# Kernel optimization log

Hardware: AMD Instinct MI355X
Metric: run time of the kernel (lower is better)

Reference implementation:

```python
import jax, jax.numpy as jnp
import numpy as np

IN_FEAT, HIDDEN, OUT_FEAT = 2048, 1024, 2048
CODEBOOK_DIM, NUM_CODES = 32, 256
B, S = 4, 4096


def setup_inputs() -> dict:
    key = jax.random.key(0)
    ks = jax.random.split(key, 10)
    sc = lambda fan_in: 1.0 / np.sqrt(fan_in)
    return {
        "x": jax.random.normal(ks[0], (B, S, IN_FEAT), dtype=jnp.float32),
        # down: Linear(in_feat, hidden)
        "down_w": jax.random.normal(ks[1], (HIDDEN, IN_FEAT), dtype=jnp.float32) * sc(IN_FEAT),
        "down_b": jax.random.normal(ks[2], (HIDDEN,), dtype=jnp.float32) * sc(IN_FEAT),
        # VQ project_in: Linear(hidden, codebook_dim)
        "pin_w": jax.random.normal(ks[3], (CODEBOOK_DIM, HIDDEN), dtype=jnp.float32) * sc(HIDDEN),
        "pin_b": jax.random.normal(ks[4], (CODEBOOK_DIM,), dtype=jnp.float32) * sc(HIDDEN),
        # codebook embeddings
        "codebook": jax.random.normal(ks[5], (NUM_CODES, CODEBOOK_DIM), dtype=jnp.float32),
        # VQ project_out: Linear(codebook_dim, hidden)
        "pout_w": jax.random.normal(ks[6], (HIDDEN, CODEBOOK_DIM), dtype=jnp.float32) * sc(CODEBOOK_DIM),
        "pout_b": jax.random.normal(ks[7], (HIDDEN,), dtype=jnp.float32) * sc(CODEBOOK_DIM),
        # up: Linear(hidden, out_feat)
        "up_w": jax.random.normal(ks[8], (OUT_FEAT, HIDDEN), dtype=jnp.float32) * sc(HIDDEN),
        "up_b": jax.random.normal(ks[9], (OUT_FEAT,), dtype=jnp.float32) * sc(HIDDEN),
    }


def reference(x, down_w, down_b, pin_w, pin_b, codebook, pout_w, pout_b, up_w, up_b):
    # down-proj: [B,S,in] -> [B,S,hidden]
    h = jnp.einsum("bsi,hi->bsh", x, down_w) + down_b
    # VQ project_in: [B,S,hidden] -> [B,S,codebook_dim]
    z = jnp.einsum("bsh,ch->bsc", h, pin_w) + pin_b
    # squared euclidean distances to codebook: [B,S,num_codes]
    dist = (
        jnp.sum(z * z, axis=-1, keepdims=True)
        - 2.0 * jnp.einsum("bsc,nc->bsn", z, codebook)
        + jnp.sum(codebook * codebook, axis=-1)
    )
    indices = jnp.argmin(dist, axis=-1)  # [B,S] int
    quant = codebook[indices]            # [B,S,codebook_dim]
    # straight-through estimator
    quant = z + jax.lax.stop_gradient(quant - z)
    # VQ project_out: -> [B,S,hidden]
    hq = jnp.einsum("bsc,hc->bsh", quant, pout_w) + pout_b
    # up-proj: -> [B,S,out]
    out = jnp.einsum("bsh,oh->bso", hq, up_w) + up_b
    commit_loss = jnp.zeros((), dtype=x.dtype)  # commitment_weight = 0
    return jnp.clip(out, -1.0, 1.0), indices, commit_loss
```

## Files before the change

### kernel.cpp

```cpp
#include <hip/hip_runtime.h>

#define TOK   16384
#define INFT  2048
#define HID   1024
#define CBD   32
#define NC    256
#define OUTF  2048
#define KB    4

#define WS_UPWT   0
#define WS_ZPART  0
#define WS_PART   2097152
#define WS_WFT    3145728
#define WS_U2C    3211264
#define WS_BF     3276800
#define WS_BPART  3278880
#define WS_T      3311648
#define WS_IDX    3835936

__global__ void kt_transpose(const float* __restrict__ up_w, float* __restrict__ up_wT) {
    __shared__ float tile[32][33];
    int h0 = blockIdx.x * 32;
    int o0 = blockIdx.y * 32;
    int tx = threadIdx.x & 31, ty = threadIdx.x >> 5;
    #pragma unroll
    for (int j = 0; j < 32; j += 8)
        tile[ty + j][tx] = up_w[(o0 + ty + j) * HID + h0 + tx];
    __syncthreads();
    #pragma unroll
    for (int j = 0; j < 32; j += 8)
        up_wT[(h0 + ty + j) * OUTF + o0 + tx] = tile[tx][ty + j];
}

__global__ void k_fuse_partial(const float* __restrict__ lhs, const float* __restrict__ rhs,
                               float* __restrict__ part, int lhsSC, int lhsSK) {
    int i  = blockIdx.x * 256 + threadIdx.x;
    int k0 = blockIdx.y * 64;
    float acc[32];
    #pragma unroll
    for (int c = 0; c < 32; c++) acc[c] = 0.f;
    #pragma unroll 4
    for (int j = 0; j < 64; j++) {
        float xv = rhs[(k0 + j) * 2048 + i];
        #pragma unroll
        for (int c = 0; c < 32; c++)
            acc[c] = fmaf(lhs[c * lhsSC + (k0 + j) * lhsSK], xv, acc[c]);
    }
    #pragma unroll
    for (int c = 0; c < 32; c++)
        part[(blockIdx.y * 32 + c) * 2048 + i] = acc[c];
}

__global__ void k_fuse_reduce(const float* __restrict__ part, float* __restrict__ outw,
                              int outSI, int outSC) {
    int f = blockIdx.x * 256 + threadIdx.x;
    int i = f & 2047, c = f >> 11;
    float s = 0.f;
    #pragma unroll
    for (int b = 0; b < 16; b++) s += part[b * 65536 + c * 2048 + i];
    outw[i * outSI + c * outSC] = s;
}

__global__ void k_bias_f(const float* __restrict__ pin_w, const float* __restrict__ pin_b,
                         const float* __restrict__ down_b, float* __restrict__ bf) {
    __shared__ float red[256];
    int c = threadIdx.x >> 3, seg = threadIdx.x & 7;
    float s = 0.f;
    #pragma unroll 8
    for (int k = seg * 128; k < seg * 128 + 128; k++)
        s = fmaf(pin_w[c * HID + k], down_b[k], s);
    red[threadIdx.x] = s;
    __syncthreads();
    if (threadIdx.x < 32) {
        float t = pin_b[threadIdx.x];
        #pragma unroll
        for (int q = 0; q < 8; q++) t += red[threadIdx.x * 8 + q];
        bf[threadIdx.x] = t;
    }
}

__global__ void k_bias2_part(const float* __restrict__ up_wT, const float* __restrict__ pout_b,
                             const float* __restrict__ up_b, float* __restrict__ bpart) {
    int o  = blockIdx.x * 256 + threadIdx.x;
    int hc = blockIdx.y;
    float s = (hc == 0) ? up_b[o] : 0.f;
    #pragma unroll 8
    for (int h = hc * 64; h < hc * 64 + 64; h++)
        s = fmaf(up_wT[h * 2048 + o], pout_b[h], s);
    bpart[hc * 2048 + o] = s;
}

__global__ void k_table(const float* __restrict__ U2c, const float* __restrict__ cb,
                        const float* __restrict__ bpart, float* __restrict__ T) {
    int n = blockIdx.x;
    int o = blockIdx.y * 256 + threadIdx.x;
    float s = 0.f;
    #pragma unroll
    for (int hc = 0; hc < 16; hc++) s += bpart[hc * 2048 + o];
    #pragma unroll
    for (int c = 0; c < 32; c++)
        s = fmaf(cb[n * 32 + c], U2c[c * 2048 + o], s);
    T[n * 2048 + o] = s;
}

__global__ __launch_bounds__(256) void k_zpart(const float* __restrict__ x,
                                               const float* __restrict__ WfT,
                                               float* __restrict__ zpart) {
    __shared__ float4 xs[64 * 33 + 1];
    int tid  = threadIdx.x;
    int lane = tid & 63;
    int w    = __builtin_amdgcn_readfirstlane(tid >> 6);
    int m0   = blockIdx.x * 64;
    int kb   = blockIdx.y;

    float acc[32];
    #pragma unroll
    for (int c = 0; c < 32; c++) acc[c] = 0.f;

    for (int sc = 0; sc < 4; sc++) {
        int k0 = kb * 512 + sc * 128;
        #pragma unroll
        for (int j = 0; j < 8; j++) {
            int f = j * 256 + tid;
            int t = f >> 5, q = f & 31;
            xs[t * 33 + q] = *(const float4*)(x + (size_t)(m0 + t) * 2048 + k0 + q * 4);
        }
        __syncthreads();
        const float* wr = WfT + (size_t)(k0 + w * 32) * 32;
        #pragma unroll 2
        for (int j = 0; j < 8; j++) {
            float4 xv = xs[lane * 33 + w * 8 + j];
            #pragma unroll
            for (int c = 0; c < 32; c++) {
                acc[c] = fmaf(wr[(j * 4 + 0) * 32 + c], xv.x, acc[c]);
                acc[c] = fmaf(wr[(j * 4 + 1) * 32 + c], xv.y, acc[c]);
                acc[c] = fmaf(wr[(j * 4 + 2) * 32 + c], xv.z, acc[c]);
                acc[c] = fmaf(wr[(j * 4 + 3) * 32 + c], xv.w, acc[c]);
            }
        }
        __syncthreads();
    }

    float* rp = (float*)xs;
    #pragma unroll
    for (int c = 0; c < 32; c++)
        rp[(w * 64 + lane) * 33 + c] = acc[c];
    __syncthreads();
    int t  = tid >> 2;
    int cq = (tid & 3) * 8;
    float s[8];
    #pragma unroll
    for (int j = 0; j < 8; j++) {
        float v = rp[(0 * 64 + t) * 33 + cq + j];
        #pragma unroll
        for (int ww = 1; ww < 4; ww++) v += rp[(ww * 64 + t) * 33 + cq + j];
        s[j] = v;
    }
    float* zp = zpart + ((size_t)kb * TOK + m0 + t) * 32 + cq;
    *(float4*)zp       = make_float4(s[0], s[1], s[2], s[3]);
    *(float4*)(zp + 4) = make_float4(s[4], s[5], s[6], s[7]);
}

__global__ __launch_bounds__(256) void k_zred(
    const float* __restrict__ zpart, const float* __restrict__ bf,
    const float* __restrict__ cb,
    int* __restrict__ idx_i, float* __restrict__ idx_f) {
    __shared__ float z_s[64 * 36];
    __shared__ float cbs[256 * 36];
    __shared__ float cbn[256];
    __shared__ float red_d[256];
    __shared__ int   red_i[256];

    int tid  = threadIdx.x;
    int lane = tid & 63;
    int w    = __builtin_amdgcn_readfirstlane(tid >> 6);
    int m0   = blockIdx.x * 64;

    #pragma unroll
    for (int i = 0; i < 8; i++) {
        int f = i * 256 + tid;
        int t = f >> 5, c = f & 31;
        float s = bf[c];
        #pragma unroll
        for (int kb = 0; kb < KB; kb++)
            s += zpart[((size_t)kb * TOK + m0 + t) * 32 + c];
        z_s[t * 36 + c] = s;
    }
    #pragma unroll
    for (int j = 0; j < 8; j++) {
        int f = j * 256 + tid;
        int n = f >> 3, q = f & 7;
        float4 v = *(const float4*)(cb + n * 32 + q * 4);
        cbs[n * 36 + q * 4 + 0] = v.x;
        cbs[n * 36 + q * 4 + 1] = v.y;
        cbs[n * 36 + q * 4 + 2] = v.z;
        cbs[n * 36 + q * 4 + 3] = v.w;
    }
    __syncthreads();
    {
        float s = 0.f;
        #pragma unroll
        for (int q = 0; q < 8; q++) {
            float4 v = *(const float4*)(&cbs[tid * 36 + q * 4]);
            s += v.x * v.x + v.y * v.y + v.z * v.z + v.w * v.w;
        }
        cbn[tid] = s;
    }
    __syncthreads();

    float z[32];
    #pragma unroll
    for (int q = 0; q < 8; q++) {
        float4 v = *(const float4*)(&z_s[lane * 36 + q * 4]);
        z[q * 4 + 0] = v.x; z[q * 4 + 1] = v.y; z[q * 4 + 2] = v.z; z[q * 4 + 3] = v.w;
    }
    float bd = 3.4e38f; int bi = 0;
    for (int t = 0; t < 64; t++) {
        int n = w * 64 + t;
        float s = 0.f;
        #pragma unroll
        for (int q = 0; q < 8; q++) {
            float4 v = *(const float4*)(&cbs[n * 36 + q * 4]);
            s = fmaf(v.x, z[q * 4 + 0], s);
            s = fmaf(v.y, z[q * 4 + 1], s);
            s = fmaf(v.z, z[q * 4 + 2], s);
            s = fmaf(v.w, z[q * 4 + 3], s);
        }
        float d = fmaf(-2.f, s, cbn[n]);
        if (d < bd) { bd = d; bi = n; }
    }
    red_d[w * 64 + lane] = bd;
    red_i[w * 64 + lane] = bi;
    __syncthreads();
    if (tid < 64) {
        float d0 = red_d[tid]; int i0 = red_i[tid];
        #pragma unroll
        for (int ww = 1; ww < 4; ww++) {
            float d1 = red_d[ww * 64 + tid];
            int   i1 = red_i[ww * 64 + tid];
            if (d1 < d0) { d0 = d1; i0 = i1; }
        }
        idx_i[m0 + tid] = i0;
        idx_f[m0 + tid] = (float)i0;
    }
}

__global__ void k_gather(const float* __restrict__ T, const int* __restrict__ idx_i,
                         float* __restrict__ out, float* __restrict__ loss) {
    int m   = blockIdx.x * 2 + (threadIdx.x >> 7);
    int sub = threadIdx.x & 127;
    int n = idx_i[m];
    const float4* Tr = (const float4*)(T + (size_t)n * 2048);
    float4* Or = (float4*)(out + (size_t)m * 2048);
    #pragma unroll
    for (int j = 0; j < 4; j++) {
        float4 v = Tr[j * 128 + sub];
        v.x = fminf(fmaxf(v.x, -1.f), 1.f);
        v.y = fminf(fmaxf(v.y, -1.f), 1.f);
        v.z = fminf(fmaxf(v.z, -1.f), 1.f);
        v.w = fminf(fmaxf(v.w, -1.f), 1.f);
        Or[j * 128 + sub] = v;
    }
    if (blockIdx.x == 0 && threadIdx.x == 0) *loss = 0.f;
}

extern "C" void kernel_launch(void* const* d_in, const int* in_sizes, int n_in,
                              void* d_out, int out_size, void* d_ws, size_t ws_size,
                              hipStream_t stream) {
    const float* x      = (const float*)d_in[0];
    const float* down_w = (const float*)d_in[1];
    const float* down_b = (const float*)d_in[2];
    const float* pin_w  = (const float*)d_in[3];
    const float* pin_b  = (const float*)d_in[4];
    const float* cb     = (const float*)d_in[5];
    const float* pout_w = (const float*)d_in[6];
    const float* pout_b = (const float*)d_in[7];
    const float* up_w   = (const float*)d_in[8];
    const float* up_b   = (const float*)d_in[9];

    float* ws    = (float*)d_ws;
    float* up_wT = ws + WS_UPWT;
    float* zpart = ws + WS_ZPART;
    float* part  = ws + WS_PART;
    float* WfT   = ws + WS_WFT;
    float* U2c   = ws + WS_U2C;
    float* bf    = ws + WS_BF;
    float* bpart = ws + WS_BPART;
    float* T     = ws + WS_T;
    int*   idx   = (int*)(ws + WS_IDX);

    float* out_f  = (float*)d_out;
    float* idx_f  = out_f + (size_t)TOK * OUTF;
    float* loss_f = idx_f + TOK;

    kt_transpose<<<dim3(32, 64), 256, 0, stream>>>(up_w, up_wT);
    k_fuse_partial<<<dim3(8, 16), 256, 0, stream>>>(pin_w, down_w, part, HID, 1);
    k_fuse_reduce<<<256, 256, 0, stream>>>(part, WfT, 32, 1);
    k_bias_f<<<1, 256, 0, stream>>>(pin_w, pin_b, down_b, bf);
    k_fuse_partial<<<dim3(8, 16), 256, 0, stream>>>(pout_w, up_wT, part, 1, CBD);
    k_fuse_reduce<<<256, 256, 0, stream>>>(part, U2c, 1, 2048);
    k_bias2_part<<<dim3(8, 16), 256, 0, stream>>>(up_wT, pout_b, up_b, bpart);
    k_table<<<dim3(256, 8), 256, 0, stream>>>(U2c, cb, bpart, T);

    k_zpart<<<dim3(256, KB), 256, 0, stream>>>(x, WfT, zpart);
    k_zred<<<256, 256, 0, stream>>>(zpart, bf, cb, idx, idx_f);
    k_gather<<<8192, 256, 0, stream>>>(T, idx, out_f, loss_f);
}
```

Before: 456.8 us.

## Merge eleven launches into four stages with block-range dispatch and fused gather

```diff
diff --git a/kernel.cpp b/kernel.cpp
--- a/kernel.cpp
+++ b/kernel.cpp
@@ -10,166 +10,209 @@
 
 #define WS_UPWT   0
 #define WS_ZPART  0
-#define WS_PART   2097152
+#define WS_PART1  2097152
+#define WS_T      2097152
 #define WS_WFT    3145728
-#define WS_U2C    3211264
-#define WS_BF     3276800
-#define WS_BPART  3278880
-#define WS_T      3311648
-#define WS_IDX    3835936
-
-__global__ void kt_transpose(const float* __restrict__ up_w, float* __restrict__ up_wT) {
-    __shared__ float tile[32][33];
-    int h0 = blockIdx.x * 32;
-    int o0 = blockIdx.y * 32;
-    int tx = threadIdx.x & 31, ty = threadIdx.x >> 5;
-    #pragma unroll
-    for (int j = 0; j < 32; j += 8)
-        tile[ty + j][tx] = up_w[(o0 + ty + j) * HID + h0 + tx];
-    __syncthreads();
-    #pragma unroll
-    for (int j = 0; j < 32; j += 8)
-        up_wT[(h0 + ty + j) * OUTF + o0 + tx] = tile[tx][ty + j];
-}
-
-__global__ void k_fuse_partial(const float* __restrict__ lhs, const float* __restrict__ rhs,
-                               float* __restrict__ part, int lhsSC, int lhsSK) {
-    int i  = blockIdx.x * 256 + threadIdx.x;
-    int k0 = blockIdx.y * 64;
-    float acc[32];
-    #pragma unroll
-    for (int c = 0; c < 32; c++) acc[c] = 0.f;
-    #pragma unroll 4
-    for (int j = 0; j < 64; j++) {
-        float xv = rhs[(k0 + j) * 2048 + i];
+#define WS_BF     3211264
+#define WS_BPART  3211296
+#define WS_PART2  3311648
+
+__global__ __launch_bounds__(256) void k_stage1(
+    const float* __restrict__ up_w, const float* __restrict__ pin_w,
+    const float* __restrict__ pin_b, const float* __restrict__ down_w,
+    const float* __restrict__ down_b, float* __restrict__ ws) {
+    int bid = blockIdx.x, tid = threadIdx.x;
+    if (bid < 2048) {
+        __shared__ float tile[32][33];
+        float* up_wT = ws + WS_UPWT;
+        int h0 = (bid & 31) * 32;
+        int o0 = (bid >> 5) * 32;
+        int tx = tid & 31, ty = tid >> 5;
+        #pragma unroll
+        for (int j = 0; j < 32; j += 8)
+            tile[ty + j][tx] = up_w[(o0 + ty + j) * HID + h0 + tx];
+        __syncthreads();
+        #pragma unroll
+        for (int j = 0; j < 32; j += 8)
+            up_wT[(h0 + ty + j) * OUTF + o0 + tx] = tile[tx][ty + j];
+    } else if (bid < 2176) {
+        float* part1 = ws + WS_PART1;
+        int b  = bid - 2048;
+        int i  = (b & 7) * 256 + tid;
+        int k0 = (b >> 3) * 64;
+        float acc[32];
+        #pragma unroll
+        for (int c = 0; c < 32; c++) acc[c] = 0.f;
+        #pragma unroll 4
+        for (int j = 0; j < 64; j++) {
+            float xv = down_w[(k0 + j) * 2048 + i];
+            #pragma unroll
+            for (int c = 0; c < 32; c++)
+                acc[c] = fmaf(pin_w[c * HID + k0 + j], xv, acc[c]);
+        }
         #pragma unroll
         for (int c = 0; c < 32; c++)
-            acc[c] = fmaf(lhs[c * lhsSC + (k0 + j) * lhsSK], xv, acc[c]);
-    }
-    #pragma unroll
-    for (int c = 0; c < 32; c++)
-        part[(blockIdx.y * 32 + c) * 2048 + i] = acc[c];
-}
-
-__global__ void k_fuse_reduce(const float* __restrict__ part, float* __restrict__ outw,
-                              int outSI, int outSC) {
-    int f = blockIdx.x * 256 + threadIdx.x;
-    int i = f & 2047, c = f >> 11;
-    float s = 0.f;
-    #pragma unroll
-    for (int b = 0; b < 16; b++) s += part[b * 65536 + c * 2048 + i];
-    outw[i * outSI + c * outSC] = s;
-}
-
-__global__ void k_bias_f(const float* __restrict__ pin_w, const float* __restrict__ pin_b,
-                         const float* __restrict__ down_b, float* __restrict__ bf) {
-    __shared__ float red[256];
-    int c = threadIdx.x >> 3, seg = threadIdx.x & 7;
-    float s = 0.f;
-    #pragma unroll 8
-    for (int k = seg * 128; k < seg * 128 + 128; k++)
-        s = fmaf(pin_w[c * HID + k], down_b[k], s);
-    red[threadIdx.x] = s;
-    __syncthreads();
-    if (threadIdx.x < 32) {
-        float t = pin_b[threadIdx.x];
-        #pragma unroll
-        for (int q = 0; q < 8; q++) t += red[threadIdx.x * 8 + q];
-        bf[threadIdx.x] = t;
-    }
-}
-
-__global__ void k_bias2_part(const float* __restrict__ up_wT, const float* __restrict__ pout_b,
-                             const float* __restrict__ up_b, float* __restrict__ bpart) {
-    int o  = blockIdx.x * 256 + threadIdx.x;
-    int hc = blockIdx.y;
-    float s = (hc == 0) ? up_b[o] : 0.f;
-    #pragma unroll 8
-    for (int h = hc * 64; h < hc * 64 + 64; h++)
-        s = fmaf(up_wT[h * 2048 + o], pout_b[h], s);
-    bpart[hc * 2048 + o] = s;
-}
-
-__global__ void k_table(const float* __restrict__ U2c, const float* __restrict__ cb,
-                        const float* __restrict__ bpart, float* __restrict__ T) {
-    int n = blockIdx.x;
-    int o = blockIdx.y * 256 + threadIdx.x;
-    float s = 0.f;
-    #pragma unroll
-    for (int hc = 0; hc < 16; hc++) s += bpart[hc * 2048 + o];
-    #pragma unroll
-    for (int c = 0; c < 32; c++)
-        s = fmaf(cb[n * 32 + c], U2c[c * 2048 + o], s);
-    T[n * 2048 + o] = s;
-}
-
-__global__ __launch_bounds__(256) void k_zpart(const float* __restrict__ x,
-                                               const float* __restrict__ WfT,
-                                               float* __restrict__ zpart) {
+            part1[((b >> 3) * 32 + c) * 2048 + i] = acc[c];
+    } else {
+        __shared__ float red[256];
+        float* bf = ws + WS_BF;
+        int c = tid >> 3, seg = tid & 7;
+        float s = 0.f;
+        #pragma unroll 8
+        for (int k = seg * 128; k < seg * 128 + 128; k++)
+            s = fmaf(pin_w[c * HID + k], down_b[k], s);
+        red[tid] = s;
+        __syncthreads();
+        if (tid < 32) {
+            float t = pin_b[tid];
+            #pragma unroll
+            for (int q = 0; q < 8; q++) t += red[tid * 8 + q];
+            bf[tid] = t;
+        }
+    }
+}
+
+__global__ __launch_bounds__(256) void k_stage2(
+    const float* __restrict__ pout_w, const float* __restrict__ pout_b,
+    const float* __restrict__ up_b, float* __restrict__ ws) {
+    int bid = blockIdx.x, tid = threadIdx.x;
+    if (bid < 256) {
+        const float* part1 = ws + WS_PART1;
+        float* WfT = ws + WS_WFT;
+        int f = bid * 256 + tid;
+        int i = f & 2047, c = f >> 11;
+        float s = 0.f;
+        #pragma unroll
+        for (int b = 0; b < 16; b++) s += part1[b * 65536 + c * 2048 + i];
+        WfT[i * 32 + c] = s;
+    } else {
+        const float* up_wT = ws + WS_UPWT;
+        float* part2 = ws + WS_PART2;
+        float* bpart = ws + WS_BPART;
+        int b  = bid - 256;
+        int i  = (b & 7) * 256 + tid;
+        int hc = b >> 3;
+        int k0 = hc * 128;
+        float acc[32];
+        #pragma unroll
+        for (int c = 0; c < 32; c++) acc[c] = 0.f;
+        float accb = 0.f;
+        #pragma unroll 4
+        for (int j = 0; j < 128; j++) {
+            float xv = up_wT[(k0 + j) * 2048 + i];
+            accb = fmaf(pout_b[k0 + j], xv, accb);
+            #pragma unroll
+            for (int c = 0; c < 32; c++)
+                acc[c] = fmaf(pout_w[(k0 + j) * 32 + c], xv, acc[c]);
+        }
+        #pragma unroll
+        for (int c = 0; c < 32; c++)
+            part2[(hc * 32 + c) * 2048 + i] = acc[c];
+        bpart[hc * 2048 + i] = accb + (hc == 0 ? up_b[i] : 0.f);
+    }
+}
+
+__global__ __launch_bounds__(256) void k_stage3(
+    const float* __restrict__ x, const float* __restrict__ cb,
+    float* __restrict__ ws) {
     __shared__ float4 xs[64 * 33 + 1];
-    int tid  = threadIdx.x;
-    int lane = tid & 63;
-    int w    = __builtin_amdgcn_readfirstlane(tid >> 6);
-    int m0   = blockIdx.x * 64;
-    int kb   = blockIdx.y;
-
-    float acc[32];
-    #pragma unroll
-    for (int c = 0; c < 32; c++) acc[c] = 0.f;
-
-    for (int sc = 0; sc < 4; sc++) {
-        int k0 = kb * 512 + sc * 128;
+    int bid = blockIdx.x, tid = threadIdx.x;
+    if (bid < 64) {
+        const float* part2 = ws + WS_PART2;
+        const float* bpart = ws + WS_BPART;
+        float* T = ws + WS_T;
+        int o  = (bid & 7) * 256 + tid;
+        int n0 = (bid >> 3) * 32;
+        float u[32];
+        #pragma unroll
+        for (int c = 0; c < 32; c++) {
+            float s = 0.f;
+            #pragma unroll
+            for (int kc = 0; kc < 8; kc++)
+                s += part2[(kc * 32 + c) * 2048 + o];
+            u[c] = s;
+        }
+        float bsum = 0.f;
+        #pragma unroll
+        for (int hc = 0; hc < 8; hc++) bsum += bpart[hc * 2048 + o];
+        for (int n = n0; n < n0 + 32; n++) {
+            float s = bsum;
+            #pragma unroll
+            for (int c = 0; c < 32; c++)
+                s = fmaf(cb[n * 32 + c], u[c], s);
+            T[n * 2048 + o] = s;
+        }
+    } else {
+        const float* WfT = ws + WS_WFT;
+        float* zpart = ws + WS_ZPART;
+        int b    = bid - 64;
+        int lane = tid & 63;
+        int w    = __builtin_amdgcn_readfirstlane(tid >> 6);
+        int m0   = (b & 255) * 64;
+        int kb   = b >> 8;
+
+        float acc[32];
+        #pragma unroll
+        for (int c = 0; c < 32; c++) acc[c] = 0.f;
+
+        for (int sc = 0; sc < 4; sc++) {
+            int k0 = kb * 512 + sc * 128;
+            #pragma unroll
+            for (int j = 0; j < 8; j++) {
+                int f = j * 256 + tid;
+                int t = f >> 5, q = f & 31;
+                xs[t * 33 + q] = *(const float4*)(x + (size_t)(m0 + t) * 2048 + k0 + q * 4);
+            }
+            __syncthreads();
+            const float* wr = WfT + (size_t)(k0 + w * 32) * 32;
+            #pragma unroll 2
+            for (int j = 0; j < 8; j++) {
+                float4 xv = xs[lane * 33 + w * 8 + j];
+                #pragma unroll
+                for (int c = 0; c < 32; c++) {
+                    acc[c] = fmaf(wr[(j * 4 + 0) * 32 + c], xv.x, acc[c]);
+                    acc[c] = fmaf(wr[(j * 4 + 1) * 32 + c], xv.y, acc[c]);
+                    acc[c] = fmaf(wr[(j * 4 + 2) * 32 + c], xv.z, acc[c]);
+                    acc[c] = fmaf(wr[(j * 4 + 3) * 32 + c], xv.w, acc[c]);
+                }
+            }
+            __syncthreads();
+        }
+
+        float* rp = (float*)xs;
+        #pragma unroll
+        for (int c = 0; c < 32; c++)
+            rp[(w * 64 + lane) * 33 + c] = acc[c];
+        __syncthreads();
+        int t  = tid >> 2;
+        int cq = (tid & 3) * 8;
+        float s[8];
         #pragma unroll
         for (int j = 0; j < 8; j++) {
-            int f = j * 256 + tid;
-            int t = f >> 5, q = f & 31;
-            xs[t * 33 + q] = *(const float4*)(x + (size_t)(m0 + t) * 2048 + k0 + q * 4);
-        }
-        __syncthreads();
-        const float* wr = WfT + (size_t)(k0 + w * 32) * 32;
-        #pragma unroll 2
-        for (int j = 0; j < 8; j++) {
-            float4 xv = xs[lane * 33 + w * 8 + j];
-            #pragma unroll
-            for (int c = 0; c < 32; c++) {
-                acc[c] = fmaf(wr[(j * 4 + 0) * 32 + c], xv.x, acc[c]);
-                acc[c] = fmaf(wr[(j * 4 + 1) * 32 + c], xv.y, acc[c]);
-                acc[c] = fmaf(wr[(j * 4 + 2) * 32 + c], xv.z, acc[c]);
-                acc[c] = fmaf(wr[(j * 4 + 3) * 32 + c], xv.w, acc[c]);
-            }
-        }
-        __syncthreads();
-    }
-
-    float* rp = (float*)xs;
-    #pragma unroll
-    for (int c = 0; c < 32; c++)
-        rp[(w * 64 + lane) * 33 + c] = acc[c];
-    __syncthreads();
-    int t  = tid >> 2;
-    int cq = (tid & 3) * 8;
-    float s[8];
-    #pragma unroll
-    for (int j = 0; j < 8; j++) {
-        float v = rp[(0 * 64 + t) * 33 + cq + j];
-        #pragma unroll
-        for (int ww = 1; ww < 4; ww++) v += rp[(ww * 64 + t) * 33 + cq + j];
-        s[j] = v;
-    }
-    float* zp = zpart + ((size_t)kb * TOK + m0 + t) * 32 + cq;
-    *(float4*)zp       = make_float4(s[0], s[1], s[2], s[3]);
-    *(float4*)(zp + 4) = make_float4(s[4], s[5], s[6], s[7]);
-}
-
-__global__ __launch_bounds__(256) void k_zred(
-    const float* __restrict__ zpart, const float* __restrict__ bf,
-    const float* __restrict__ cb,
-    int* __restrict__ idx_i, float* __restrict__ idx_f) {
+            float v = rp[(0 * 64 + t) * 33 + cq + j];
+            #pragma unroll
+            for (int ww = 1; ww < 4; ww++) v += rp[(ww * 64 + t) * 33 + cq + j];
+            s[j] = v;
+        }
+        float* zp = zpart + ((size_t)kb * TOK + m0 + t) * 32 + cq;
+        *(float4*)zp       = make_float4(s[0], s[1], s[2], s[3]);
+        *(float4*)(zp + 4) = make_float4(s[4], s[5], s[6], s[7]);
+    }
+}
+
+__global__ __launch_bounds__(256) void k_stage4(
+    const float* __restrict__ cb, const float* __restrict__ ws,
+    float* __restrict__ out, float* __restrict__ idx_f, float* __restrict__ loss) {
     __shared__ float z_s[64 * 36];
     __shared__ float cbs[256 * 36];
     __shared__ float cbn[256];
     __shared__ float red_d[256];
     __shared__ int   red_i[256];
+    __shared__ int   idx_s[64];
+
+    const float* zpart = ws + WS_ZPART;
+    const float* bf    = ws + WS_BF;
+    const float* T     = ws + WS_T;
 
     int tid  = threadIdx.x;
     int lane = tid & 63;
@@ -240,28 +283,31 @@
             int   i1 = red_i[ww * 64 + tid];
             if (d1 < d0) { d0 = d1; i0 = i1; }
         }
-        idx_i[m0 + tid] = i0;
+        idx_s[tid] = i0;
         idx_f[m0 + tid] = (float)i0;
     }
-}
-
-__global__ void k_gather(const float* __restrict__ T, const int* __restrict__ idx_i,
-                         float* __restrict__ out, float* __restrict__ loss) {
-    int m   = blockIdx.x * 2 + (threadIdx.x >> 7);
-    int sub = threadIdx.x & 127;
-    int n = idx_i[m];
-    const float4* Tr = (const float4*)(T + (size_t)n * 2048);
-    float4* Or = (float4*)(out + (size_t)m * 2048);
-    #pragma unroll
-    for (int j = 0; j < 4; j++) {
-        float4 v = Tr[j * 128 + sub];
-        v.x = fminf(fmaxf(v.x, -1.f), 1.f);
-        v.y = fminf(fmaxf(v.y, -1.f), 1.f);
-        v.z = fminf(fmaxf(v.z, -1.f), 1.f);
-        v.w = fminf(fmaxf(v.w, -1.f), 1.f);
-        Or[j * 128 + sub] = v;
-    }
-    if (blockIdx.x == 0 && threadIdx.x == 0) *loss = 0.f;
+    __syncthreads();
+
+    const float4* T4 = (const float4*)T;
+    float4* O4 = (float4*)(out + (size_t)m0 * 2048);
+    #pragma unroll 2
+    for (int r = 0; r < 64; r++) {
+        int n = idx_s[r];
+        const float4* Tr = T4 + (size_t)n * 512;
+        float4 v0 = Tr[tid];
+        float4 v1 = Tr[256 + tid];
+        v0.x = fminf(fmaxf(v0.x, -1.f), 1.f);
+        v0.y = fminf(fmaxf(v0.y, -1.f), 1.f);
+        v0.z = fminf(fmaxf(v0.z, -1.f), 1.f);
+        v0.w = fminf(fmaxf(v0.w, -1.f), 1.f);
+        v1.x = fminf(fmaxf(v1.x, -1.f), 1.f);
+        v1.y = fminf(fmaxf(v1.y, -1.f), 1.f);
+        v1.z = fminf(fmaxf(v1.z, -1.f), 1.f);
+        v1.w = fminf(fmaxf(v1.w, -1.f), 1.f);
+        O4[(size_t)r * 512 + tid]       = v0;
+        O4[(size_t)r * 512 + 256 + tid] = v1;
+    }
+    if (blockIdx.x == 0 && tid == 0) *loss = 0.f;
 }
 
 extern "C" void kernel_launch(void* const* d_in, const int* in_sizes, int n_in,
@@ -278,31 +324,13 @@
     const float* up_w   = (const float*)d_in[8];
     const float* up_b   = (const float*)d_in[9];
 
-    float* ws    = (float*)d_ws;
-    float* up_wT = ws + WS_UPWT;
-    float* zpart = ws + WS_ZPART;
-    float* part  = ws + WS_PART;
-    float* WfT   = ws + WS_WFT;
-    float* U2c   = ws + WS_U2C;
-    float* bf    = ws + WS_BF;
-    float* bpart = ws + WS_BPART;
-    float* T     = ws + WS_T;
-    int*   idx   = (int*)(ws + WS_IDX);
-
+    float* ws = (float*)d_ws;
     float* out_f  = (float*)d_out;
     float* idx_f  = out_f + (size_t)TOK * OUTF;
     float* loss_f = idx_f + TOK;
 
-    kt_transpose<<<dim3(32, 64), 256, 0, stream>>>(up_w, up_wT);
-    k_fuse_partial<<<dim3(8, 16), 256, 0, stream>>>(pin_w, down_w, part, HID, 1);
-    k_fuse_reduce<<<256, 256, 0, stream>>>(part, WfT, 32, 1);
-    k_bias_f<<<1, 256, 0, stream>>>(pin_w, pin_b, down_b, bf);
-    k_fuse_partial<<<dim3(8, 16), 256, 0, stream>>>(pout_w, up_wT, part, 1, CBD);
-    k_fuse_reduce<<<256, 256, 0, stream>>>(part, U2c, 1, 2048);
-    k_bias2_part<<<dim3(8, 16), 256, 0, stream>>>(up_wT, pout_b, up_b, bpart);
-    k_table<<<dim3(256, 8), 256, 0, stream>>>(U2c, cb, bpart, T);
-
-    k_zpart<<<dim3(256, KB), 256, 0, stream>>>(x, WfT, zpart);
-    k_zred<<<256, 256, 0, stream>>>(zpart, bf, cb, idx, idx_f);
-    k_gather<<<8192, 256, 0, stream>>>(T, idx, out_f, loss_f);
-}
+    k_stage1<<<2177, 256, 0, stream>>>(up_w, pin_w, pin_b, down_w, down_b, ws);
+    k_stage2<<<320,  256, 0, stream>>>(pout_w, pout_b, up_b, ws);
+    k_stage3<<<1088, 256, 0, stream>>>(x, cb, ws);
+    k_stage4<<<256,  256, 0, stream>>>(cb, ws, out_f, idx_f, loss_f);
+}
```

New measurement: 391.3 us. 14.3% less time.
